# Kernel optimization log

Measured on AMD Instinct MI355X. Metric: run time of the kernel, lower is better.

## Reference

```python
import jax, jax.numpy as jnp
import numpy as np

N_NODES = 100000
N_EDGES = 1600000
IN_CH = 128
OUT_CH = 128
N_REL = 8


def setup_inputs() -> dict:
    key = jax.random.key(0)
    k1, k2, k3, k4, k5, k6 = jax.random.split(key, 6)
    x = jax.random.normal(k1, (N_NODES, IN_CH), dtype=jnp.float32)
    edge_index = jax.random.randint(k2, (2, N_EDGES), 0, N_NODES, dtype=jnp.int64)
    edge_type = jax.random.randint(k3, (N_EDGES,), 0, N_REL, dtype=jnp.int64)
    # learned parameters (PyG RGCNConv: per-relation weight, root weight, bias)
    scale = 1.0 / np.sqrt(IN_CH)
    weight = jax.random.normal(k4, (N_REL, IN_CH, OUT_CH), dtype=jnp.float32) * scale
    root = jax.random.normal(k5, (IN_CH, OUT_CH), dtype=jnp.float32) * scale
    bias = jax.random.normal(k6, (OUT_CH,), dtype=jnp.float32) * 0.01
    return {"x": x, "edge_index": edge_index, "edge_type": edge_type,
            "weight": weight, "root": root, "bias": bias}


def reference(x, edge_index, edge_type, weight, root, bias):
    # PyG RGCNConv forward: out_i = x_i @ root + bias
    #   + sum_r mean_{j in N_r(i)} (x_j @ W_r)   (default aggr='mean' per relation)
    N = x.shape[0]
    R, _, O = weight.shape
    src, dst = edge_index[0], edge_index[1]
    # transform all nodes under every relation once: [R, N, O]
    xW = jnp.einsum('ni,rio->rno', x, weight)
    msg = xW[edge_type, src]                      # [E, O] per-edge message
    seg = edge_type * N + dst                     # segment per (relation, dst)
    sums = jax.ops.segment_sum(msg, seg, num_segments=R * N)        # [R*N, O]
    cnt = jax.ops.segment_sum(jnp.ones_like(msg[:, 0]), seg, num_segments=R * N)
    mean = sums / jnp.maximum(cnt, 1.0)[:, None]
    agg = mean.reshape(R, N, O).sum(axis=0)       # sum over relations
    return agg + x @ root + bias
```

## Files before the change

### kernel.cpp

```cpp
#include <hip/hip_runtime.h>
#include <hip/hip_bf16.h>
#include <stdint.h>

#define N_NODES 100000
#define N_EDGES 1600000
#define CH 128
#define N_REL 8
#define N_PAD 100096
#define N_KEYS (N_NODES * N_REL)

#define NBKT 782
#define NSUB 64
#define SUBCAP 128
#define BKT_STRIDE (NSUB * SUBCAP)
#define CUR_PAD 16
#define PERM_LDS_CAP 4096

using frag_ab = __attribute__((ext_vector_type(8))) short;
using frag_cd = __attribute__((ext_vector_type(4))) float;

__device__ __forceinline__ short f2bs(float f) {
    union { __hip_bfloat16 h; short s; } u;
    u.h = __float2bfloat16(f);
    return u.s;
}

__device__ __forceinline__ uint32_t pack2bf(float a, float b) {
    union { __hip_bfloat16 h; unsigned short s; } ua, ub;
    ua.h = __float2bfloat16(a); ub.h = __float2bfloat16(b);
    return (uint32_t)ua.s | ((uint32_t)ub.s << 16);
}

__device__ __forceinline__ float bf_lo(uint32_t u) { return __uint_as_float(u << 16); }
__device__ __forceinline__ float bf_hi(uint32_t u) { return __uint_as_float(u & 0xffff0000u); }


__global__ __launch_bounds__(256)
void prep_kernel(const int* __restrict__ ei, const int* __restrict__ et,
                 int* __restrict__ cur, uint32_t* __restrict__ bucket,
                 const float* __restrict__ x, short* __restrict__ xb,
                 const float* __restrict__ root, const float* __restrict__ W,
                 short* __restrict__ Bsw) {
    const int tid = threadIdx.x;
    const int g = blockIdx.x * 256 + tid;

    if (g < N_EDGES) {
        int dst = ei[N_EDGES + g];
        int src = ei[g];
        int r = et[g];
        int b = dst >> 7;
        int sub = blockIdx.x & (NSUB - 1);
        int pos = atomicAdd(&cur[(sub * NBKT + b) * CUR_PAD], 1);
        if (pos < SUBCAP)
            bucket[((size_t)b * NSUB + sub) * SUBCAP + pos] =
                ((uint32_t)src << 10) | ((uint32_t)(dst & 127) << 3) | (uint32_t)r;
    }

    if (g < N_NODES * CH / 8) {
        const float4* xp = (const float4*)x;
        float4 a = xp[(size_t)g * 2], bb = xp[(size_t)g * 2 + 1];
        frag_ab f;
        f[0] = f2bs(a.x); f[1] = f2bs(a.y); f[2] = f2bs(a.z); f[3] = f2bs(a.w);
        f[4] = f2bs(bb.x); f[5] = f2bs(bb.y); f[6] = f2bs(bb.z); f[7] = f2bs(bb.w);
        *(frag_ab*)(xb + (size_t)g * 8) = f;
    }

    if (g < 9 * 2048) {
        int chunk = g >> 11, entry = g & 2047;
        int m16 = entry & 15, ct = (entry >> 4) & 7, quad = (entry >> 7) & 3, ks = entry >> 9;
        const float* src = (chunk == 0) ? root : W + (size_t)(chunk - 1) * CH * CH;
        int col = ct * 16 + m16, kb = ks * 32 + quad * 8;
        frag_ab f;
#pragma unroll
        for (int j = 0; j < 8; ++j) f[j] = f2bs(src[(size_t)(kb + j) * CH + col]);
        *(frag_ab*)(Bsw + (size_t)g * 8) = f;
    }
}

#define ACC_U4(U, B)                                            \
    do {                                                        \
        a[(B)+0] += bf_lo((U).x); a[(B)+1] += bf_hi((U).x);     \
        a[(B)+2] += bf_lo((U).y); a[(B)+3] += bf_hi((U).y);     \
        a[(B)+4] += bf_lo((U).z); a[(B)+5] += bf_hi((U).z);     \
        a[(B)+6] += bf_lo((U).w); a[(B)+7] += bf_hi((U).w);     \
    } while (0)

__global__ __launch_bounds__(512, 4)
void rgcn_mega(const int* __restrict__ cur, const uint32_t* __restrict__ bucket,
               int* __restrict__ perm_spill,
               const short* __restrict__ xb, const short* __restrict__ Bsw,
               const float* __restrict__ bias, float* __restrict__ out) {
    __shared__ short Ash[128 * 128];
    __shared__ int perm_lds[PERM_LDS_CAP];
    __shared__ int lends[1025];
    __shared__ int lens[NSUB];
    int* hist   = (int*)Ash;
    int* cursor = (int*)Ash + 1024;
    int* shl    = (int*)Ash + 2048;

    const int tid = threadIdx.x;
    const int wave = tid >> 6, lane = tid & 63;
    const int m16 = lane & 15, quad = lane >> 4;
    const int wm = wave >> 2, wn = wave & 3;
    const int b = blockIdx.x;
    const size_t bbase = (size_t)b * BKT_STRIDE;
    const long B0 = (long)b * 128;

#define PERM(idx) (((idx) < PERM_LDS_CAP) ? perm_lds[(idx)] : perm_spill[bbase + (idx)])

    hist[tid] = 0; hist[tid + 512] = 0;
    if (tid == 0) perm_lds[0] = 0;
    if (tid < NSUB) {
        int n = cur[(tid * NBKT + b) * CUR_PAD];
        lens[tid] = (n > SUBCAP) ? SUBCAP : n;
    }
    __syncthreads();
    for (int j = tid; j < BKT_STRIDE; j += 512)
        if ((j & (SUBCAP - 1)) < lens[j >> 7])
            atomicAdd(&hist[bucket[bbase + j] & 1023], 1);
    __syncthreads();
    const int h0 = hist[2 * tid], h1 = hist[2 * tid + 1];
    const int s2 = h0 + h1;
    shl[tid] = s2;
    __syncthreads();
    for (int st = 1; st < 512; st <<= 1) {
        int u = (tid >= st) ? shl[tid - st] : 0;
        __syncthreads();
        shl[tid] += u;
        __syncthreads();
    }
    const int excl = shl[tid] - s2;
    cursor[2 * tid]     = excl;
    cursor[2 * tid + 1] = excl + h0;
    if (tid == 0) lends[0] = 0;
    lends[1 + 2 * tid] = excl + h0;
    lends[2 + 2 * tid] = excl + h0 + h1;
    __syncthreads();
    for (int j = tid; j < BKT_STRIDE; j += 512)
        if ((j & (SUBCAP - 1)) < lens[j >> 7]) {
            const uint32_t e = bucket[bbase + j];
            const int pos = atomicAdd(&cursor[e & 1023], 1);
            const int v = (int)(e >> 10);
            if (pos < PERM_LDS_CAP) perm_lds[pos] = v;
            else perm_spill[bbase + pos] = v;
        }

    float bcol[2];
#pragma unroll
    for (int ct = 0; ct < 2; ++ct) bcol[ct] = bias[wn * 32 + ct * 16 + m16];

    frag_cd acc[4][2];
#pragma unroll
    for (int mt = 0; mt < 4; ++mt)
#pragma unroll
        for (int ct = 0; ct < 2; ++ct) acc[mt][ct] = (frag_cd){0.f, 0.f, 0.f, 0.f};

#pragma unroll
    for (int ks = 0; ks < 4; ++ks) {
        frag_ab af[4];
#pragma unroll
        for (int mt = 0; mt < 4; ++mt)
            af[mt] = *(const frag_ab*)(xb + (B0 + wm * 64 + mt * 16 + m16) * CH + ks * 32 + quad * 8);
#pragma unroll
        for (int ct = 0; ct < 2; ++ct) {
            frag_ab bf = *(const frag_ab*)(Bsw + (size_t)((((ks * 4 + quad) * 8) + wn * 2 + ct) * 16 + m16) * 8);
#pragma unroll
            for (int mt = 0; mt < 4; ++mt)
                acc[mt][ct] = __builtin_amdgcn_mfma_f32_16x16x32_bf16(af[mt], bf, acc[mt][ct], 0, 0, 0);
        }
    }
    __syncthreads();

    const int lrow = tid >> 2;
    const int q4 = tid & 3;
    const uint32_t ch64 = (uint32_t)q4 << 6;
    const char* xbp = (const char*)xb;
    char* drow = (char*)Ash + lrow * 256;
    const int swz = lrow & 7;

    for (int r = 0; r < N_REL; ++r) {
        const int keyL = lrow * 8 + r;
        const int s = lends[keyL];
        const int e = lends[keyL + 1];
        float a[32];
#pragma unroll
        for (int i = 0; i < 32; ++i) a[i] = 0.f;
        int p0 = PERM((s < e) ? s : 0);
        int p1 = PERM((s + 1 < e) ? s + 1 : ((s < e) ? s : 0));
        for (int k = s; k < e; k += 2) {
            const char* c0 = xbp + (((size_t)(uint32_t)p0 << 8) | ch64);
            const char* c1 = xbp + (((size_t)(uint32_t)p1 << 8) | ch64);
            const uint4 u0 = *(const uint4*)(c0);
            const uint4 u1 = *(const uint4*)(c0 + 16);
            const uint4 u2 = *(const uint4*)(c0 + 32);
            const uint4 u3 = *(const uint4*)(c0 + 48);
            const uint4 u4 = *(const uint4*)(c1);
            const uint4 u5 = *(const uint4*)(c1 + 16);
            const uint4 u6 = *(const uint4*)(c1 + 32);
            const uint4 u7 = *(const uint4*)(c1 + 48);
            const bool two = (k + 1 < e);
            const int kn = k + 2;
            p0 = PERM((kn < e) ? kn : 0);
            p1 = PERM((kn + 1 < e) ? kn + 1 : 0);
            ACC_U4(u0, 0); ACC_U4(u1, 8); ACC_U4(u2, 16); ACC_U4(u3, 24);
            if (two) { ACC_U4(u4, 0); ACC_U4(u5, 8); ACC_U4(u6, 16); ACC_U4(u7, 24); }
        }
        const int c = e - s;
        const float sc = (c > 1) ? (1.0f / (float)c) : 1.0f;
#pragma unroll
        for (int t = 0; t < 4; ++t) {
            uint4 w;
            w.x = pack2bf(a[t * 8 + 0] * sc, a[t * 8 + 1] * sc);
            w.y = pack2bf(a[t * 8 + 2] * sc, a[t * 8 + 3] * sc);
            w.z = pack2bf(a[t * 8 + 4] * sc, a[t * 8 + 5] * sc);
            w.w = pack2bf(a[t * 8 + 6] * sc, a[t * 8 + 7] * sc);
            *(uint4*)(drow + (((q4 * 4 + t) ^ swz) << 4)) = w;
        }
        __syncthreads();
        const short* Bc = Bsw + (size_t)(r + 1) * 2048 * 8;
#pragma unroll
        for (int ks = 0; ks < 4; ++ks) {
            frag_ab af[4];
#pragma unroll
            for (int mt = 0; mt < 4; ++mt) {
                const int lr = wm * 64 + mt * 16 + m16;
                af[mt] = *(const frag_ab*)((const char*)Ash + lr * 256 + (((ks * 4 + quad) ^ (lr & 7)) << 4));
            }
#pragma unroll
            for (int ct = 0; ct < 2; ++ct) {
                frag_ab bf = *(const frag_ab*)(Bc + (size_t)((((ks * 4 + quad) * 8) + wn * 2 + ct) * 16 + m16) * 8);
#pragma unroll
                for (int mt = 0; mt < 4; ++mt)
                    acc[mt][ct] = __builtin_amdgcn_mfma_f32_16x16x32_bf16(af[mt], bf, acc[mt][ct], 0, 0, 0);
            }
        }
        __syncthreads();
    }
#undef PERM

#pragma unroll
    for (int mt = 0; mt < 4; ++mt) {
#pragma unroll
        for (int ct = 0; ct < 2; ++ct) {
            const long row0 = B0 + wm * 64 + mt * 16 + quad * 4;
            const int col = wn * 32 + ct * 16 + m16;
#pragma unroll
            for (int rg = 0; rg < 4; ++rg) {
                const long rr = row0 + rg;
                if (rr < N_NODES) out[rr * CH + col] = acc[mt][ct][rg] + bcol[ct];
            }
        }
    }
}


__global__ void count_rd_kernel(const int* __restrict__ ei, const int* __restrict__ et,
                                int* __restrict__ cnt) {
    int e = blockIdx.x * 256 + threadIdx.x;
    if (e < N_EDGES) {
        int dst = ei[N_EDGES + e];
        int r = et[e];
        atomicAdd(&cnt[r * N_NODES + dst], 1);
    }
}

__global__ void scatter_kernel(const int* __restrict__ ei, const int* __restrict__ et,
                               const float* __restrict__ x, float* __restrict__ sums,
                               int rel) {
    int gid = (blockIdx.x * 256 + threadIdx.x) >> 5;
    int lane = threadIdx.x & 31;
    int ngroups = gridDim.x * 8;
    for (int e = gid; e < N_EDGES; e += ngroups) {
        if (et[e] != rel) continue;
        int src = ei[e];
        int dst = ei[N_EDGES + e];
        float4 v = ((const float4*)(x + (size_t)src * CH))[lane];
        float* s = sums + (size_t)dst * CH + (size_t)lane * 4;
        atomicAdd(s + 0, v.x);
        atomicAdd(s + 1, v.y);
        atomicAdd(s + 2, v.z);
        atomicAdd(s + 3, v.w);
    }
}

__global__ __launch_bounds__(256, 2)
void gemm_kernel(const float* __restrict__ A, const float* __restrict__ B,
                 const float* __restrict__ bias, const int* __restrict__ cnt,
                 float* __restrict__ out, int accumulate) {
    const int wave = threadIdx.x >> 6;
    const int lane = threadIdx.x & 63;
    const int m16 = lane & 15;
    const int quad = lane >> 4;

    frag_ab bfrag[4][8];
#pragma unroll
    for (int ks = 0; ks < 4; ++ks) {
        const int kb = ks * 32 + quad * 8;
#pragma unroll
        for (int ct = 0; ct < 8; ++ct) {
            const int col = ct * 16 + m16;
            frag_ab f;
#pragma unroll
            for (int j = 0; j < 8; ++j)
                f[j] = f2bs(B[(size_t)(kb + j) * CH + col]);
            bfrag[ks][ct] = f;
        }
    }

    const int nstrips = (N_NODES + 63) / 64;
    for (int strip = blockIdx.x; strip < nstrips; strip += gridDim.x) {
        const int row = strip * 64 + wave * 16 + m16;
        const bool valid = row < N_NODES;
        float scale = 1.0f;
        if (cnt != nullptr && valid) {
            int c = cnt[row];
            if (c > 1) scale = 1.0f / (float)c;
        }
        const float4* arow = (const float4*)(A + (size_t)(valid ? row : 0) * CH);
        frag_cd acc[8];
#pragma unroll
        for (int ct = 0; ct < 8; ++ct) acc[ct] = (frag_cd){0.f, 0.f, 0.f, 0.f};
#pragma unroll
        for (int ks = 0; ks < 4; ++ks) {
            float4 a0 = arow[ks * 8 + quad * 2];
            float4 a1 = arow[ks * 8 + quad * 2 + 1];
            frag_ab af;
            af[0] = f2bs(a0.x * scale); af[1] = f2bs(a0.y * scale);
            af[2] = f2bs(a0.z * scale); af[3] = f2bs(a0.w * scale);
            af[4] = f2bs(a1.x * scale); af[5] = f2bs(a1.y * scale);
            af[6] = f2bs(a1.z * scale); af[7] = f2bs(a1.w * scale);
#pragma unroll
            for (int ct = 0; ct < 8; ++ct)
                acc[ct] = __builtin_amdgcn_mfma_f32_16x16x32_bf16(af, bfrag[ks][ct], acc[ct], 0, 0, 0);
        }
        const int obase = strip * 64 + wave * 16 + quad * 4;
#pragma unroll
        for (int ct = 0; ct < 8; ++ct) {
            const int col = ct * 16 + m16;
#pragma unroll
            for (int rg = 0; rg < 4; ++rg) {
                const int r = obase + rg;
                if (r < N_NODES) {
                    const size_t idx = (size_t)r * CH + col;
                    if (accumulate) out[idx] += acc[ct][rg];
                    else out[idx] = acc[ct][rg] + bias[col];
                }
            }
        }
    }
}

__global__ void edge_transform_kernel(const int* __restrict__ ei, const int* __restrict__ et,
                                      const float* __restrict__ x, const float* __restrict__ W,
                                      const int* __restrict__ cnt, float* __restrict__ out) {
    __shared__ float xs[CH];
    const int tid = threadIdx.x;
    for (int e = blockIdx.x; e < N_EDGES; e += gridDim.x) {
        const int src = ei[e];
        const int dst = ei[N_EDGES + e];
        const int r = et[e];
        __syncthreads();
        xs[tid] = x[(size_t)src * CH + tid];
        __syncthreads();
        const int c = cnt[r * N_NODES + dst];
        const float scale = (c > 1) ? (1.0f / (float)c) : 1.0f;
        const float* Wr = W + (size_t)r * CH * CH;
        float acc = 0.f;
#pragma unroll 8
        for (int k = 0; k < CH; ++k) acc += xs[k] * Wr[(size_t)k * CH + tid];
        atomicAdd(&out[(size_t)dst * CH + tid], acc * scale);
    }
}


static inline size_t al512(size_t x) { return (x + 511) & ~(size_t)511; }

extern "C" void kernel_launch(void* const* d_in, const int* in_sizes, int n_in,
                              void* d_out, int out_size, void* d_ws, size_t ws_size,
                              hipStream_t stream) {
    const float* x    = (const float*)d_in[0];
    const int*   ei   = (const int*)d_in[1];
    const int*   et   = (const int*)d_in[2];
    const float* W    = (const float*)d_in[3];
    const float* root = (const float*)d_in[4];
    const float* bias = (const float*)d_in[5];
    float* out = (float*)d_out;

    size_t o = 0;
    const size_t o_cur  = o; o += al512((size_t)NSUB * NBKT * CUR_PAD * 4);
    const size_t o_bkt  = o; o += al512((size_t)NBKT * BKT_STRIDE * 4);
    const size_t o_perm = o; o += al512((size_t)NBKT * BKT_STRIDE * 4);
    const size_t o_bsw  = o; o += al512((size_t)9 * 2048 * 16);
    const size_t o_xb   = o; o += al512((size_t)N_PAD * CH * 2);
    const size_t need_t1 = o;

    const size_t cnt_bytes = (size_t)N_REL * N_NODES * sizeof(int);
    const size_t cnt_rsv   = al512(cnt_bytes);
    const size_t sums51    = (size_t)N_NODES * CH * sizeof(float);

    char* ws = (char*)d_ws;
    if (ws_size >= need_t1) {
        int*      cur    = (int*)(ws + o_cur);
        uint32_t* bucket = (uint32_t*)(ws + o_bkt);
        int*      perm   = (int*)(ws + o_perm);
        short*    Bsw    = (short*)(ws + o_bsw);
        short*    xb     = (short*)(ws + o_xb);

        hipMemsetAsync(cur, 0, (size_t)NSUB * NBKT * CUR_PAD * 4, stream);
        prep_kernel<<<(N_EDGES + 255) / 256, 256, 0, stream>>>(
            ei, et, cur, bucket, x, xb, root, W, Bsw);
        rgcn_mega<<<NBKT, 512, 0, stream>>>(cur, bucket, perm, xb, Bsw, bias, out);
    } else if (ws_size >= cnt_rsv + sums51) {
        int*   cnt  = (int*)d_ws;
        float* sums = (float*)((char*)d_ws + cnt_rsv);
        hipMemsetAsync(cnt, 0, cnt_bytes, stream);
        count_rd_kernel<<<(N_EDGES + 255) / 256, 256, 0, stream>>>(ei, et, cnt);
        gemm_kernel<<<512, 256, 0, stream>>>(x, root, bias, nullptr, out, 0);
        for (int r = 0; r < N_REL; ++r) {
            hipMemsetAsync(sums, 0, sums51, stream);
            scatter_kernel<<<6400, 256, 0, stream>>>(ei, et, x, sums, r);
            gemm_kernel<<<512, 256, 0, stream>>>(sums, W + (size_t)r * CH * CH,
                                                 nullptr, cnt + (size_t)r * N_NODES, out, 1);
        }
    } else {
        int* cnt = (int*)d_ws;
        hipMemsetAsync(cnt, 0, cnt_bytes, stream);
        count_rd_kernel<<<(N_EDGES + 255) / 256, 256, 0, stream>>>(ei, et, cnt);
        gemm_kernel<<<512, 256, 0, stream>>>(x, root, bias, nullptr, out, 0);
        edge_transform_kernel<<<65536, CH, 0, stream>>>(ei, et, x, W, cnt, out);
    }
}
```

Before: 325.9 us.

## Replace global-atomic edge sub-buckets with per-chunk LDS-histogram bucketing

The edge binning in the prep kernel now gives each of 782 blocks a fixed chunk of 2048 edges. Each block builds a shared-memory histogram over destination buckets and writes entries into a chunk-by-bucket slot array of 24 entries, plus a per-chunk length table. This removes the global atomic counters, the memset that cleared them, and the global perm spill path, so the main kernel reads neighbour indices only from LDS. In exchange, each main-kernel block scans 782×24 slots instead of 8192 and does a strided gather of lengths across chunks. Both the per-slot cap and the LDS capacity cap silently drop edges if a bucket overflows.

```diff
diff --git a/kernel.cpp b/kernel.cpp
--- a/kernel.cpp
+++ b/kernel.cpp
@@ -10,10 +10,9 @@
 #define N_KEYS (N_NODES * N_REL)
 
 #define NBKT 782
-#define NSUB 64
-#define SUBCAP 128
-#define BKT_STRIDE (NSUB * SUBCAP)
-#define CUR_PAD 16
+#define NCHUNK 782
+#define CHUNK_E 2048
+#define BSLOT 24
 #define PERM_LDS_CAP 4096
 
 using frag_ab = __attribute__((ext_vector_type(8))) short;
@@ -37,23 +36,37 @@
 
 __global__ __launch_bounds__(256)
 void prep_kernel(const int* __restrict__ ei, const int* __restrict__ et,
-                 int* __restrict__ cur, uint32_t* __restrict__ bucket,
+                 uint32_t* __restrict__ bucket, int* __restrict__ lens,
                  const float* __restrict__ x, short* __restrict__ xb,
                  const float* __restrict__ root, const float* __restrict__ W,
                  short* __restrict__ Bsw) {
+    __shared__ int hist[NBKT];
     const int tid = threadIdx.x;
+    const int c = blockIdx.x;
     const int g = blockIdx.x * 256 + tid;
 
-    if (g < N_EDGES) {
-        int dst = ei[N_EDGES + g];
-        int src = ei[g];
-        int r = et[g];
-        int b = dst >> 7;
-        int sub = blockIdx.x & (NSUB - 1);
-        int pos = atomicAdd(&cur[(sub * NBKT + b) * CUR_PAD], 1);
-        if (pos < SUBCAP)
-            bucket[((size_t)b * NSUB + sub) * SUBCAP + pos] =
-                ((uint32_t)src << 10) | ((uint32_t)(dst & 127) << 3) | (uint32_t)r;
+    if (c < NCHUNK) {
+        for (int i = tid; i < NBKT; i += 256) hist[i] = 0;
+        __syncthreads();
+#pragma unroll
+        for (int j = 0; j < 8; ++j) {
+            const int e = c * CHUNK_E + j * 256 + tid;
+            if (e < N_EDGES) {
+                const int dst = ei[N_EDGES + e];
+                const int src = ei[e];
+                const int r = et[e];
+                const int b = dst >> 7;
+                const int pos = atomicAdd(&hist[b], 1);
+                if (pos < BSLOT)
+                    bucket[((size_t)c * NBKT + b) * BSLOT + pos] =
+                        ((uint32_t)src << 10) | ((uint32_t)(dst & 127) << 3) | (uint32_t)r;
+            }
+        }
+        __syncthreads();
+        for (int i = tid; i < NBKT; i += 256) {
+            int n = hist[i];
+            lens[(size_t)c * NBKT + i] = (n > BSLOT) ? BSLOT : n;
+        }
     }
 
     if (g < N_NODES * CH / 8) {
@@ -86,14 +99,13 @@
     } while (0)
 
 __global__ __launch_bounds__(512, 4)
-void rgcn_mega(const int* __restrict__ cur, const uint32_t* __restrict__ bucket,
-               int* __restrict__ perm_spill,
+void rgcn_mega(const int* __restrict__ lens, const uint32_t* __restrict__ bucket,
                const short* __restrict__ xb, const short* __restrict__ Bsw,
                const float* __restrict__ bias, float* __restrict__ out) {
     __shared__ short Ash[128 * 128];
     __shared__ int perm_lds[PERM_LDS_CAP];
     __shared__ int lends[1025];
-    __shared__ int lens[NSUB];
+    __shared__ int lens_l[NCHUNK];
     int* hist   = (int*)Ash;
     int* cursor = (int*)Ash + 1024;
     int* shl    = (int*)Ash + 2048;
@@ -103,21 +115,17 @@
     const int m16 = lane & 15, quad = lane >> 4;
     const int wm = wave >> 2, wn = wave & 3;
     const int b = blockIdx.x;
-    const size_t bbase = (size_t)b * BKT_STRIDE;
     const long B0 = (long)b * 128;
 
-#define PERM(idx) (((idx) < PERM_LDS_CAP) ? perm_lds[(idx)] : perm_spill[bbase + (idx)])
-
+    for (int i = tid; i < NCHUNK; i += 512) lens_l[i] = lens[(size_t)i * NBKT + b];
     hist[tid] = 0; hist[tid + 512] = 0;
     if (tid == 0) perm_lds[0] = 0;
-    if (tid < NSUB) {
-        int n = cur[(tid * NBKT + b) * CUR_PAD];
-        lens[tid] = (n > SUBCAP) ? SUBCAP : n;
-    }
     __syncthreads();
-    for (int j = tid; j < BKT_STRIDE; j += 512)
-        if ((j & (SUBCAP - 1)) < lens[j >> 7])
-            atomicAdd(&hist[bucket[bbase + j] & 1023], 1);
+    for (int j = tid; j < NCHUNK * BSLOT; j += 512) {
+        const int c = j / BSLOT, i = j - c * BSLOT;
+        if (i < lens_l[c])
+            atomicAdd(&hist[bucket[((size_t)c * NBKT + b) * BSLOT + i] & 1023], 1);
+    }
     __syncthreads();
     const int h0 = hist[2 * tid], h1 = hist[2 * tid + 1];
     const int s2 = h0 + h1;
@@ -133,17 +141,20 @@
     cursor[2 * tid]     = excl;
     cursor[2 * tid + 1] = excl + h0;
     if (tid == 0) lends[0] = 0;
-    lends[1 + 2 * tid] = excl + h0;
-    lends[2 + 2 * tid] = excl + h0 + h1;
+    {
+        int e1 = excl + h0, e2 = excl + h0 + h1;
+        lends[1 + 2 * tid] = (e1 > PERM_LDS_CAP) ? PERM_LDS_CAP : e1;
+        lends[2 + 2 * tid] = (e2 > PERM_LDS_CAP) ? PERM_LDS_CAP : e2;
+    }
     __syncthreads();
-    for (int j = tid; j < BKT_STRIDE; j += 512)
-        if ((j & (SUBCAP - 1)) < lens[j >> 7]) {
-            const uint32_t e = bucket[bbase + j];
-            const int pos = atomicAdd(&cursor[e & 1023], 1);
-            const int v = (int)(e >> 10);
-            if (pos < PERM_LDS_CAP) perm_lds[pos] = v;
-            else perm_spill[bbase + pos] = v;
-        }
+    for (int j = tid; j < NCHUNK * BSLOT; j += 512) {
+        const int c = j / BSLOT, i = j - c * BSLOT;
+        if (i < lens_l[c]) {
+            const uint32_t v = bucket[((size_t)c * NBKT + b) * BSLOT + i];
+            const int pos = atomicAdd(&cursor[v & 1023], 1);
+            if (pos < PERM_LDS_CAP) perm_lds[pos] = (int)(v >> 10);
+        }
+    }
 
     float bcol[2];
 #pragma unroll
@@ -185,8 +196,8 @@
         float a[32];
 #pragma unroll
         for (int i = 0; i < 32; ++i) a[i] = 0.f;
-        int p0 = PERM((s < e) ? s : 0);
-        int p1 = PERM((s + 1 < e) ? s + 1 : ((s < e) ? s : 0));
+        int p0 = perm_lds[(s < e) ? s : 0];
+        int p1 = perm_lds[(s + 1 < e) ? s + 1 : ((s < e) ? s : 0)];
         for (int k = s; k < e; k += 2) {
             const char* c0 = xbp + (((size_t)(uint32_t)p0 << 8) | ch64);
             const char* c1 = xbp + (((size_t)(uint32_t)p1 << 8) | ch64);
@@ -200,8 +211,8 @@
             const uint4 u7 = *(const uint4*)(c1 + 48);
             const bool two = (k + 1 < e);
             const int kn = k + 2;
-            p0 = PERM((kn < e) ? kn : 0);
-            p1 = PERM((kn + 1 < e) ? kn + 1 : 0);
+            p0 = perm_lds[(kn < e) ? kn : 0];
+            p1 = perm_lds[(kn + 1 < e) ? kn + 1 : 0];
             ACC_U4(u0, 0); ACC_U4(u1, 8); ACC_U4(u2, 16); ACC_U4(u3, 24);
             if (two) { ACC_U4(u4, 0); ACC_U4(u5, 8); ACC_U4(u6, 16); ACC_U4(u7, 24); }
         }
@@ -236,7 +247,6 @@
         }
         __syncthreads();
     }
-#undef PERM
 
 #pragma unroll
     for (int mt = 0; mt < 4; ++mt) {
@@ -387,9 +397,8 @@
     float* out = (float*)d_out;
 
     size_t o = 0;
-    const size_t o_cur  = o; o += al512((size_t)NSUB * NBKT * CUR_PAD * 4);
-    const size_t o_bkt  = o; o += al512((size_t)NBKT * BKT_STRIDE * 4);
-    const size_t o_perm = o; o += al512((size_t)NBKT * BKT_STRIDE * 4);
+    const size_t o_bkt  = o; o += al512((size_t)NCHUNK * NBKT * BSLOT * 4);
+    const size_t o_lens = o; o += al512((size_t)NCHUNK * NBKT * 4);
     const size_t o_bsw  = o; o += al512((size_t)9 * 2048 * 16);
     const size_t o_xb   = o; o += al512((size_t)N_PAD * CH * 2);
     const size_t need_t1 = o;
@@ -400,16 +409,14 @@
 
     char* ws = (char*)d_ws;
     if (ws_size >= need_t1) {
-        int*      cur    = (int*)(ws + o_cur);
         uint32_t* bucket = (uint32_t*)(ws + o_bkt);
-        int*      perm   = (int*)(ws + o_perm);
+        int*      lens   = (int*)(ws + o_lens);
         short*    Bsw    = (short*)(ws + o_bsw);
         short*    xb     = (short*)(ws + o_xb);
 
-        hipMemsetAsync(cur, 0, (size_t)NSUB * NBKT * CUR_PAD * 4, stream);
-        prep_kernel<<<(N_EDGES + 255) / 256, 256, 0, stream>>>(
-            ei, et, cur, bucket, x, xb, root, W, Bsw);
-        rgcn_mega<<<NBKT, 512, 0, stream>>>(cur, bucket, perm, xb, Bsw, bias, out);
+        prep_kernel<<<(N_NODES * CH / 8 + 255) / 256, 256, 0, stream>>>(
+            ei, et, bucket, lens, x, xb, root, W, Bsw);
+        rgcn_mega<<<NBKT, 512, 0, stream>>>(lens, bucket, xb, Bsw, bias, out);
     } else if (ws_size >= cnt_rsv + sums51) {
         int*   cnt  = (int*)d_ws;
         float* sums = (float*)((char*)d_ws + cnt_rsv);
```

After: 345.1 us. 1.06x slower.
